# Kernel tuning notes

Hardware: AMD Instinct MI355X
Metric: run time of the kernel (lower is better)

The kernel has to match this reference:

```python
import jax, jax.numpy as jnp
from jax import lax
import numpy as np

SEQ, BATCH, HID = 1024, 2048, 64

def setup_inputs() -> dict:
    key = jax.random.key(0)
    ks = jax.random.split(key, 9)
    s = 1.0 / np.sqrt(HID)
    return {
        "x": jax.random.normal(ks[0], (SEQ, BATCH), dtype=jnp.float32),
        "W_ih": jax.random.uniform(ks[1], (4 * HID, 1), jnp.float32, -s, s),
        "W_hh": jax.random.uniform(ks[2], (4 * HID, HID), jnp.float32, -s, s),
        "b_ih": jax.random.uniform(ks[3], (4 * HID,), jnp.float32, -s, s),
        "b_hh": jax.random.uniform(ks[4], (4 * HID,), jnp.float32, -s, s),
        "fc1_w": jax.random.uniform(ks[5], (128, HID), jnp.float32, -s, s),
        "fc1_b": jax.random.uniform(ks[6], (128,), jnp.float32, -s, s),
        "fc2_w": jax.random.uniform(ks[7], (5, 128), jnp.float32, -s, s),
        "fc2_b": jax.random.uniform(ks[8], (5,), jnp.float32, -s, s),
    }

def reference(x, W_ih, W_hh, b_ih, b_hh, fc1_w, fc1_b, fc2_w, fc2_b):
    # x: (S, B) -> unsqueeze(2) gives (S, B, 1); input_size == 1 so the input
    # projection is an outer product, precomputed for all timesteps at once.
    # gx: (S, B, 4H), gate order i, f, g, o (PyTorch convention)
    gx = x[:, :, None] * W_ih[:, 0][None, None, :] + b_ih

    B = x.shape[1]
    h0 = jnp.zeros((B, HID), dtype=x.dtype)
    c0 = jnp.zeros((B, HID), dtype=x.dtype)

    def step(carry, g):
        h, c = carry
        gates = g + h @ W_hh.T + b_hh  # (B, 4H)
        i, f, gg, o = jnp.split(gates, 4, axis=-1)
        i = jax.nn.sigmoid(i)
        f = jax.nn.sigmoid(f)
        gg = jnp.tanh(gg)
        o = jax.nn.sigmoid(o)
        c = f * c + i * gg
        h = o * jnp.tanh(c)
        return (h, c), None

    (h_n, c_n), _ = lax.scan(step, (h0, c0), gx)
    # Original uses hidden[1] == cell state c_n for the MLP head (no activation).
    out = (c_n @ fc1_w.T + fc1_b) @ fc2_w.T + fc2_b  # (B, 5)
    return out
```

## Files before the change

### kernel.cpp

```cpp
#include <hip/hip_runtime.h>
#include <hip/hip_bf16.h>

#define S_LEN 1024
#define BATCH 2048
#define HID   64
#define MB    4
#define NBLK  (BATCH / MB)
#define NTHR  (MB * HID)

typedef _Float16 half8 __attribute__((ext_vector_type(8)));
typedef float    f32x4 __attribute__((ext_vector_type(4)));
typedef float    f32x4a __attribute__((ext_vector_type(4))) __attribute__((aligned(16)));

#define L2E 1.4426950408889634f
#define HSTRIDE 72

__global__ __launch_bounds__(NTHR, 2) void lstm_kernel(
    const float* __restrict__ x,
    const float* __restrict__ W_ih,
    const float* __restrict__ W_hh,
    const float* __restrict__ b_ih,
    const float* __restrict__ b_hh,
    const float* __restrict__ fc1_w,
    const float* __restrict__ fc1_b,
    const float* __restrict__ fc2_w,
    const float* __restrict__ fc2_b,
    float* __restrict__ out)
{
    __shared__ __align__(16) float    xs[S_LEN * MB];
    __shared__ __align__(16) _Float16 h_buf[2][MB * HSTRIDE];
    __shared__ __align__(16) float    head_lds[MB * HID + MB * 128];

    const int tid  = threadIdx.x;
    const int lane = tid & 63;
    const int wave = tid >> 6;
    const int l15  = lane & 15;
    const int quad = lane >> 4;
    const int b0   = blockIdx.x * MB;

    {
        float4* xs4 = (float4*)xs;
        #pragma unroll
        for (int t = 0; t < 4; ++t) {
            const int s = tid + 256 * t;
            xs4[s] = *(const float4*)(x + (size_t)s * BATCH + b0);
        }
    }

    {
        unsigned* hz = (unsigned*)&h_buf[0][0];
        for (int i = tid; i < 2 * MB * HSTRIDE / 2; i += NTHR) hz[i] = 0u;
    }

    half8 wfrag[4][2];
    #pragma unroll
    for (int g = 0; g < 4; ++g) {
        const float s = (g == 2) ? (-2.0f * L2E) : (-L2E);
        const float* wr = W_hh + (g * 64 + 16 * wave + l15) * HID + quad * 8;
        #pragma unroll
        for (int kt = 0; kt < 2; ++kt) {
            half8 f;
            #pragma unroll
            for (int j = 0; j < 8; ++j) f[j] = (_Float16)(wr[kt * 32 + j] * s);
            wfrag[g][kt] = f;
        }
    }

    const int u = 16 * wave + l15;
    float wih_s[4], bias_s[4];
    #pragma unroll
    for (int g = 0; g < 4; ++g) {
        const int n = g * 64 + u;
        const float s = (g == 2) ? (-2.0f * L2E) : (-L2E);
        wih_s[g]  = W_ih[n] * s;
        bias_s[g] = (b_ih[n] + b_hh[n]) * s;
    }

    float c = 0.0f;
    const f32x4 zero4 = {0.f, 0.f, 0.f, 0.f};

    const _Float16* a0p = &h_buf[0][0] + (l15 >> 2) * HSTRIDE + quad * 8;
    const _Float16* a1p = &h_buf[1][0] + (l15 >> 2) * HSTRIDE + quad * 8;
    _Float16* w0p = &h_buf[0][0] + quad * HSTRIDE + u;
    _Float16* w1p = &h_buf[1][0] + quad * HSTRIDE + u;
    const float* xp = xs + quad;

    __syncthreads();

    auto body = [&](int s, const _Float16* ar, _Float16* hw) {
        const float xv = xp[4 * s];

        half8 a0 = *(const half8*)(ar);
        half8 a1 = *(const half8*)(ar + 32);

        f32x4 acc[4];
        #pragma unroll
        for (int g = 0; g < 4; ++g) {
            acc[g] = __builtin_amdgcn_mfma_f32_16x16x32_f16(a0, wfrag[g][0], zero4, 0, 0, 0);
            acc[g] = __builtin_amdgcn_mfma_f32_16x16x32_f16(a1, wfrag[g][1], acc[g], 0, 0, 0);
        }

        const float gi = acc[0][0] + __builtin_fmaf(xv, wih_s[0], bias_s[0]);
        const float gf = acc[1][0] + __builtin_fmaf(xv, wih_s[1], bias_s[1]);
        const float gg = acc[2][0] + __builtin_fmaf(xv, wih_s[2], bias_s[2]);
        const float go = acc[3][0] + __builtin_fmaf(xv, wih_s[3], bias_s[3]);

        const float i_ = __builtin_amdgcn_rcpf(1.0f + __builtin_amdgcn_exp2f(gi));
        const float f_ = __builtin_amdgcn_rcpf(1.0f + __builtin_amdgcn_exp2f(gf));
        const float g_ = 2.0f * __builtin_amdgcn_rcpf(1.0f + __builtin_amdgcn_exp2f(gg)) - 1.0f;
        const float o_ = __builtin_amdgcn_rcpf(1.0f + __builtin_amdgcn_exp2f(go));

        c = f_ * c + i_ * g_;
        const float th = 2.0f * __builtin_amdgcn_rcpf(
                             1.0f + __builtin_amdgcn_exp2f((-2.0f * L2E) * c)) - 1.0f;
        const float h = o_ * th;

        hw[0] = (_Float16)h;
        __syncthreads();
    };

    for (int s = 0; s < S_LEN; s += 2) {
        body(s,     a0p, w1p);
        body(s + 1, a1p, w0p);
    }

    float* c_lds  = head_lds;
    float* h1_lds = head_lds + MB * HID;
    c_lds[quad * HID + u] = c;
    __syncthreads();

    for (int idx = tid; idx < MB * 128; idx += NTHR) {
        const int b = idx >> 7, j = idx & 127;
        const float* wrow = fc1_w + j * HID;
        const float* crow = c_lds + b * HID;
        float acc = fc1_b[j];
        #pragma unroll
        for (int k = 0; k < HID; k += 4)
            acc += crow[k] * wrow[k] + crow[k+1] * wrow[k+1]
                 + crow[k+2] * wrow[k+2] + crow[k+3] * wrow[k+3];
        h1_lds[idx] = acc;
    }
    __syncthreads();

    if (tid < MB * 5) {
        const int b = tid / 5, q = tid % 5;
        const float* wrow = fc2_w + q * 128;
        const float* hrow = h1_lds + b * 128;
        float acc = fc2_b[q];
        #pragma unroll 4
        for (int j = 0; j < 128; ++j) acc += hrow[j] * wrow[j];
        out[(b0 + b) * 5 + q] = acc;
    }
}

extern "C" void kernel_launch(void* const* d_in, const int* in_sizes, int n_in,
                              void* d_out, int out_size, void* d_ws, size_t ws_size,
                              hipStream_t stream) {
    const float* x     = (const float*)d_in[0];
    const float* W_ih  = (const float*)d_in[1];
    const float* W_hh  = (const float*)d_in[2];
    const float* b_ih  = (const float*)d_in[3];
    const float* b_hh  = (const float*)d_in[4];
    const float* fc1_w = (const float*)d_in[5];
    const float* fc1_b = (const float*)d_in[6];
    const float* fc2_w = (const float*)d_in[7];
    const float* fc2_b = (const float*)d_in[8];
    float* out = (float*)d_out;

    lstm_kernel<<<NBLK, NTHR, 0, stream>>>(x, W_ih, W_hh, b_ih, b_hh,
                                           fc1_w, fc1_b, fc2_w, fc2_b, out);
}
```

Baseline: 335.0 us.

## Halve batch per block to two sequences, doubling MFMA tiles per wave

Reduces the per-block batch from 4 to 2, so each block has 2 waves and 1024 blocks are launched instead of 512. Each wave now covers 32 hidden units with two MFMA tile sets per gate, and lanes select the accumulator matching their half. The aim is to shorten the per-step barrier across fewer waves and add more independent blocks to hide the serial recurrence latency. In exchange each wave issues twice the MFMAs per step, and the MFMA rows are even more underused, since only 2 of 16 rows hold real batch data.

After: 520.8 us. 1.55x slower.

```diff
diff --git a/kernel.cpp b/kernel.cpp
--- a/kernel.cpp
+++ b/kernel.cpp
@@ -4,13 +4,12 @@
 #define S_LEN 1024
 #define BATCH 2048
 #define HID   64
-#define MB    4
+#define MB    2
 #define NBLK  (BATCH / MB)
 #define NTHR  (MB * HID)
 
 typedef _Float16 half8 __attribute__((ext_vector_type(8)));
 typedef float    f32x4 __attribute__((ext_vector_type(4)));
-typedef float    f32x4a __attribute__((ext_vector_type(4))) __attribute__((aligned(16)));
 
 #define L2E 1.4426950408889634f
 #define HSTRIDE 72
@@ -39,11 +38,11 @@
     const int b0   = blockIdx.x * MB;
 
     {
-        float4* xs4 = (float4*)xs;
+        float2* xs2 = (float2*)xs;
         #pragma unroll
-        for (int t = 0; t < 4; ++t) {
-            const int s = tid + 256 * t;
-            xs4[s] = *(const float4*)(x + (size_t)s * BATCH + b0);
+        for (int t = 0; t < 8; ++t) {
+            const int s = tid + 128 * t;
+            xs2[s] = *(const float2*)(x + (size_t)s * BATCH + b0);
         }
     }
 
@@ -52,21 +51,26 @@
         for (int i = tid; i < 2 * MB * HSTRIDE / 2; i += NTHR) hz[i] = 0u;
     }
 
-    half8 wfrag[4][2];
+    half8 wfrag[4][2][2];
     #pragma unroll
     for (int g = 0; g < 4; ++g) {
         const float s = (g == 2) ? (-2.0f * L2E) : (-L2E);
-        const float* wr = W_hh + (g * 64 + 16 * wave + l15) * HID + quad * 8;
         #pragma unroll
-        for (int kt = 0; kt < 2; ++kt) {
-            half8 f;
+        for (int h2 = 0; h2 < 2; ++h2) {
+            const float* wr = W_hh + (g * 64 + 32 * wave + 16 * h2 + l15) * HID + quad * 8;
             #pragma unroll
-            for (int j = 0; j < 8; ++j) f[j] = (_Float16)(wr[kt * 32 + j] * s);
-            wfrag[g][kt] = f;
+            for (int kt = 0; kt < 2; ++kt) {
+                half8 f;
+                #pragma unroll
+                for (int j = 0; j < 8; ++j) f[j] = (_Float16)(wr[kt * 32 + j] * s);
+                wfrag[g][h2][kt] = f;
+            }
         }
     }
 
-    const int u = 16 * wave + l15;
+    const int bb = quad >> 1;
+    const int hh = quad & 1;
+    const int u  = 32 * wave + 16 * hh + l15;
     float wih_s[4], bias_s[4];
     #pragma unroll
     for (int g = 0; g < 4; ++g) {
@@ -79,31 +83,34 @@
     float c = 0.0f;
     const f32x4 zero4 = {0.f, 0.f, 0.f, 0.f};
 
-    const _Float16* a0p = &h_buf[0][0] + (l15 >> 2) * HSTRIDE + quad * 8;
-    const _Float16* a1p = &h_buf[1][0] + (l15 >> 2) * HSTRIDE + quad * 8;
-    _Float16* w0p = &h_buf[0][0] + quad * HSTRIDE + u;
-    _Float16* w1p = &h_buf[1][0] + quad * HSTRIDE + u;
-    const float* xp = xs + quad;
+    const _Float16* a0p = &h_buf[0][0] + (l15 >> 3) * HSTRIDE + quad * 8;
+    const _Float16* a1p = &h_buf[1][0] + (l15 >> 3) * HSTRIDE + quad * 8;
+    _Float16* w0p = &h_buf[0][0] + bb * HSTRIDE + u;
+    _Float16* w1p = &h_buf[1][0] + bb * HSTRIDE + u;
+    const float* xp = xs + bb;
 
     __syncthreads();
 
     auto body = [&](int s, const _Float16* ar, _Float16* hw) {
-        const float xv = xp[4 * s];
+        const float xv = xp[2 * s];
 
         half8 a0 = *(const half8*)(ar);
         half8 a1 = *(const half8*)(ar + 32);
 
-        f32x4 acc[4];
+        f32x4 acc[4][2];
         #pragma unroll
         for (int g = 0; g < 4; ++g) {
-            acc[g] = __builtin_amdgcn_mfma_f32_16x16x32_f16(a0, wfrag[g][0], zero4, 0, 0, 0);
-            acc[g] = __builtin_amdgcn_mfma_f32_16x16x32_f16(a1, wfrag[g][1], acc[g], 0, 0, 0);
+            #pragma unroll
+            for (int h2 = 0; h2 < 2; ++h2) {
+                acc[g][h2] = __builtin_amdgcn_mfma_f32_16x16x32_f16(a0, wfrag[g][h2][0], zero4,      0, 0, 0);
+                acc[g][h2] = __builtin_amdgcn_mfma_f32_16x16x32_f16(a1, wfrag[g][h2][1], acc[g][h2], 0, 0, 0);
+            }
         }
 
-        const float gi = acc[0][0] + __builtin_fmaf(xv, wih_s[0], bias_s[0]);
-        const float gf = acc[1][0] + __builtin_fmaf(xv, wih_s[1], bias_s[1]);
-        const float gg = acc[2][0] + __builtin_fmaf(xv, wih_s[2], bias_s[2]);
-        const float go = acc[3][0] + __builtin_fmaf(xv, wih_s[3], bias_s[3]);
+        const float gi = (hh ? acc[0][1][0] : acc[0][0][0]) + __builtin_fmaf(xv, wih_s[0], bias_s[0]);
+        const float gf = (hh ? acc[1][1][0] : acc[1][0][0]) + __builtin_fmaf(xv, wih_s[1], bias_s[1]);
+        const float gg = (hh ? acc[2][1][0] : acc[2][0][0]) + __builtin_fmaf(xv, wih_s[2], bias_s[2]);
+        const float go = (hh ? acc[3][1][0] : acc[3][0][0]) + __builtin_fmaf(xv, wih_s[3], bias_s[3]);
 
         const float i_ = __builtin_amdgcn_rcpf(1.0f + __builtin_amdgcn_exp2f(gi));
         const float f_ = __builtin_amdgcn_rcpf(1.0f + __builtin_amdgcn_exp2f(gf));
@@ -126,7 +133,7 @@
 
     float* c_lds  = head_lds;
     float* h1_lds = head_lds + MB * HID;
-    c_lds[quad * HID + u] = c;
+    c_lds[bb * HID + u] = c;
     __syncthreads();
 
     for (int idx = tid; idx < MB * 128; idx += NTHR) {
```

## Process two independent 4-row batch groups per block to interleave LSTM steps

Applied to the files above, without the earlier changes.

Each block now handles 8 batch rows as two independent 4-row groups with separate h buffers and cell states. Each thread advances both groups before a shared barrier, so there is one barrier per two group-steps and the two MFMA/transcendental chains can overlap. Block count halves and launch bounds drop to one block per SIMD-occupancy hint, which trades occupancy for instruction-level parallelism within a wave.

Result: slower. 482.5 us (+44.0%).

```diff
diff --git a/kernel.cpp b/kernel.cpp
--- a/kernel.cpp
+++ b/kernel.cpp
@@ -4,18 +4,17 @@
 #define S_LEN 1024
 #define BATCH 2048
 #define HID   64
-#define MB    4
+#define MB    8
 #define NBLK  (BATCH / MB)
-#define NTHR  (MB * HID)
+#define NTHR  256
 
 typedef _Float16 half8 __attribute__((ext_vector_type(8)));
 typedef float    f32x4 __attribute__((ext_vector_type(4)));
-typedef float    f32x4a __attribute__((ext_vector_type(4))) __attribute__((aligned(16)));
 
 #define L2E 1.4426950408889634f
-#define HSTRIDE 72
+#define HSTRIDE 80
 
-__global__ __launch_bounds__(NTHR, 2) void lstm_kernel(
+__global__ __launch_bounds__(NTHR, 1) void lstm_kernel(
     const float* __restrict__ x,
     const float* __restrict__ W_ih,
     const float* __restrict__ W_hh,
@@ -28,7 +27,7 @@
     float* __restrict__ out)
 {
     __shared__ __align__(16) float    xs[S_LEN * MB];
-    __shared__ __align__(16) _Float16 h_buf[2][MB * HSTRIDE];
+    __shared__ __align__(16) _Float16 h_buf[2][2][4 * HSTRIDE];
     __shared__ __align__(16) float    head_lds[MB * HID + MB * 128];
 
     const int tid  = threadIdx.x;
@@ -41,15 +40,16 @@
     {
         float4* xs4 = (float4*)xs;
         #pragma unroll
-        for (int t = 0; t < 4; ++t) {
-            const int s = tid + 256 * t;
-            xs4[s] = *(const float4*)(x + (size_t)s * BATCH + b0);
+        for (int t = 0; t < 8; ++t) {
+            const int idx = tid + 256 * t;
+            const int s = idx >> 1, half = idx & 1;
+            xs4[idx] = *(const float4*)(x + (size_t)s * BATCH + b0 + 4 * half);
         }
     }
 
     {
-        unsigned* hz = (unsigned*)&h_buf[0][0];
-        for (int i = tid; i < 2 * MB * HSTRIDE / 2; i += NTHR) hz[i] = 0u;
+        unsigned* hz = (unsigned*)&h_buf[0][0][0];
+        for (int i = tid; i < 2 * 2 * 4 * HSTRIDE / 2; i += NTHR) hz[i] = 0u;
     }
 
     half8 wfrag[4][2];
@@ -76,20 +76,21 @@
         bias_s[g] = (b_ih[n] + b_hh[n]) * s;
     }
 
-    float c = 0.0f;
+    float cX = 0.0f, cY = 0.0f;
     const f32x4 zero4 = {0.f, 0.f, 0.f, 0.f};
 
-    const _Float16* a0p = &h_buf[0][0] + (l15 >> 2) * HSTRIDE + quad * 8;
-    const _Float16* a1p = &h_buf[1][0] + (l15 >> 2) * HSTRIDE + quad * 8;
-    _Float16* w0p = &h_buf[0][0] + quad * HSTRIDE + u;
-    _Float16* w1p = &h_buf[1][0] + quad * HSTRIDE + u;
-    const float* xp = xs + quad;
+    const int aoff = (l15 >> 2) * HSTRIDE + quad * 8;
+    const int woff = quad * HSTRIDE + u;
+    const _Float16* aX[2] = { &h_buf[0][0][0] + aoff, &h_buf[0][1][0] + aoff };
+    const _Float16* aY[2] = { &h_buf[1][0][0] + aoff, &h_buf[1][1][0] + aoff };
+    _Float16* wX[2] = { &h_buf[0][0][0] + woff, &h_buf[0][1][0] + woff };
+    _Float16* wY[2] = { &h_buf[1][0][0] + woff, &h_buf[1][1][0] + woff };
+    const float* xpX = xs + quad;
+    const float* xpY = xs + 4 + quad;
 
     __syncthreads();
 
-    auto body = [&](int s, const _Float16* ar, _Float16* hw) {
-        const float xv = xp[4 * s];
-
+    auto body = [&](float xv, const _Float16* ar, _Float16* hw, float& c) {
         half8 a0 = *(const half8*)(ar);
         half8 a1 = *(const half8*)(ar + 32);
 
@@ -114,19 +115,22 @@
         const float th = 2.0f * __builtin_amdgcn_rcpf(
                              1.0f + __builtin_amdgcn_exp2f((-2.0f * L2E) * c)) - 1.0f;
         const float h = o_ * th;
-
         hw[0] = (_Float16)h;
-        __syncthreads();
     };
 
     for (int s = 0; s < S_LEN; s += 2) {
-        body(s,     a0p, w1p);
-        body(s + 1, a1p, w0p);
+        body(xpX[8 * s], aX[0], wX[1], cX);
+        body(xpY[8 * s], aY[0], wY[1], cY);
+        __syncthreads();
+        body(xpX[8 * (s + 1)], aX[1], wX[0], cX);
+        body(xpY[8 * (s + 1)], aY[1], wY[0], cY);
+        __syncthreads();
     }
 
     float* c_lds  = head_lds;
     float* h1_lds = head_lds + MB * HID;
-    c_lds[quad * HID + u] = c;
+    c_lds[quad * HID + u]       = cX;
+    c_lds[(4 + quad) * HID + u] = cY;
     __syncthreads();
 
     for (int idx = tid; idx < MB * 128; idx += NTHR) {
```

## Process eight batch rows per block with two wave groups sharing MFMA tiles

Applied to the files above, without the earlier changes.

Doubles the batch rows per block from 4 to 8 and the threads to 512. The two groups of four waves each pick a different accumulator element from the same 16x16 MFMA output, so each MFMA tile now covers 8 real batch rows instead of 4. The intent is to halve the number of blocks and the sequential-step work per batch row. The cost is larger blocks that synchronise 512 threads every step, and each wave still issues the same MFMAs, so the matrix work is duplicated across the wave groups.

New measurement: 389.9 us. 16.4% more time.

```diff
diff --git a/kernel.cpp b/kernel.cpp
--- a/kernel.cpp
+++ b/kernel.cpp
@@ -4,16 +4,15 @@
 #define S_LEN 1024
 #define BATCH 2048
 #define HID   64
-#define MB    4
+#define MB    8
 #define NBLK  (BATCH / MB)
-#define NTHR  (MB * HID)
+#define NTHR  512
 
 typedef _Float16 half8 __attribute__((ext_vector_type(8)));
 typedef float    f32x4 __attribute__((ext_vector_type(4)));
-typedef float    f32x4a __attribute__((ext_vector_type(4))) __attribute__((aligned(16)));
 
 #define L2E 1.4426950408889634f
-#define HSTRIDE 72
+#define HSTRIDE 80
 
 __global__ __launch_bounds__(NTHR, 2) void lstm_kernel(
     const float* __restrict__ x,
@@ -34,6 +33,8 @@
     const int tid  = threadIdx.x;
     const int lane = tid & 63;
     const int wave = tid >> 6;
+    const int ws   = wave & 3;
+    const int bh   = wave >> 2;
     const int l15  = lane & 15;
     const int quad = lane >> 4;
     const int b0   = blockIdx.x * MB;
@@ -42,8 +43,9 @@
         float4* xs4 = (float4*)xs;
         #pragma unroll
         for (int t = 0; t < 4; ++t) {
-            const int s = tid + 256 * t;
-            xs4[s] = *(const float4*)(x + (size_t)s * BATCH + b0);
+            const int idx = tid + 512 * t;
+            const int s = idx >> 1, half = idx & 1;
+            xs4[idx] = *(const float4*)(x + (size_t)s * BATCH + b0 + 4 * half);
         }
     }
 
@@ -56,7 +58,7 @@
     #pragma unroll
     for (int g = 0; g < 4; ++g) {
         const float s = (g == 2) ? (-2.0f * L2E) : (-L2E);
-        const float* wr = W_hh + (g * 64 + 16 * wave + l15) * HID + quad * 8;
+        const float* wr = W_hh + (g * 64 + 16 * ws + l15) * HID + quad * 8;
         #pragma unroll
         for (int kt = 0; kt < 2; ++kt) {
             half8 f;
@@ -66,7 +68,8 @@
         }
     }
 
-    const int u = 16 * wave + l15;
+    const int bb = 2 * quad + bh;
+    const int u  = 16 * ws + l15;
     float wih_s[4], bias_s[4];
     #pragma unroll
     for (int g = 0; g < 4; ++g) {
@@ -79,16 +82,18 @@
     float c = 0.0f;
     const f32x4 zero4 = {0.f, 0.f, 0.f, 0.f};
 
-    const _Float16* a0p = &h_buf[0][0] + (l15 >> 2) * HSTRIDE + quad * 8;
-    const _Float16* a1p = &h_buf[1][0] + (l15 >> 2) * HSTRIDE + quad * 8;
-    _Float16* w0p = &h_buf[0][0] + quad * HSTRIDE + u;
-    _Float16* w1p = &h_buf[1][0] + quad * HSTRIDE + u;
-    const float* xp = xs + quad;
+    const int aoff = (l15 >> 1) * HSTRIDE + quad * 8;
+    const _Float16* a0p = &h_buf[0][0] + aoff;
+    const _Float16* a1p = &h_buf[1][0] + aoff;
+    _Float16* w0p = &h_buf[0][0] + bb * HSTRIDE + u;
+    _Float16* w1p = &h_buf[1][0] + bb * HSTRIDE + u;
+    const float* xp = xs + bb;
+    const bool hi = (bh != 0);
 
     __syncthreads();
 
     auto body = [&](int s, const _Float16* ar, _Float16* hw) {
-        const float xv = xp[4 * s];
+        const float xv = xp[8 * s];
 
         half8 a0 = *(const half8*)(ar);
         half8 a1 = *(const half8*)(ar + 32);
@@ -100,10 +105,10 @@
             acc[g] = __builtin_amdgcn_mfma_f32_16x16x32_f16(a1, wfrag[g][1], acc[g], 0, 0, 0);
         }
 
-        const float gi = acc[0][0] + __builtin_fmaf(xv, wih_s[0], bias_s[0]);
-        const float gf = acc[1][0] + __builtin_fmaf(xv, wih_s[1], bias_s[1]);
-        const float gg = acc[2][0] + __builtin_fmaf(xv, wih_s[2], bias_s[2]);
-        const float go = acc[3][0] + __builtin_fmaf(xv, wih_s[3], bias_s[3]);
+        const float gi = (hi ? acc[0][2] : acc[0][0]) + __builtin_fmaf(xv, wih_s[0], bias_s[0]);
+        const float gf = (hi ? acc[1][2] : acc[1][0]) + __builtin_fmaf(xv, wih_s[1], bias_s[1]);
+        const float gg = (hi ? acc[2][2] : acc[2][0]) + __builtin_fmaf(xv, wih_s[2], bias_s[2]);
+        const float go = (hi ? acc[3][2] : acc[3][0]) + __builtin_fmaf(xv, wih_s[3], bias_s[3]);
 
         const float i_ = __builtin_amdgcn_rcpf(1.0f + __builtin_amdgcn_exp2f(gi));
         const float f_ = __builtin_amdgcn_rcpf(1.0f + __builtin_amdgcn_exp2f(gf));
@@ -126,7 +131,7 @@
 
     float* c_lds  = head_lds;
     float* h1_lds = head_lds + MB * HID;
-    c_lds[quad * HID + u] = c;
+    c_lds[bb * HID + u] = c;
     __syncthreads();
 
     for (int idx = tid; idx < MB * 128; idx += NTHR) {
```
